# Kernel tuning notes

Hardware: AMD Instinct MI355X
Metric: run time of the kernel (lower is better)

Reference implementation:

```python
import jax, jax.numpy as jnp
import numpy as np

N, K, D_IN, D_OUT = 50000, 32, 128, 128
TEMPERATURE = 1.0


def setup_inputs() -> dict:
    key = jax.random.key(0)
    k1, k2, k3 = jax.random.split(key, 3)
    feat = jax.random.normal(k1, (N, D_IN), dtype=jnp.float32)
    # Glorot-like scale so pairwise distances stay in a reasonable softmax range
    weight = jax.random.normal(k2, (D_IN, D_OUT), dtype=jnp.float32) / np.sqrt(D_IN)
    bias = jnp.zeros((D_OUT,), dtype=jnp.float32)
    # norm='none' -> unit edge weights; fixed-degree-k graph -> topk returns all k neighbors
    top_k_weights = jnp.ones((N, K), dtype=jnp.float32)
    top_k_idx = jax.random.randint(k3, (N, K), 0, N, dtype=jnp.int64)
    return {"feat": feat, "weight": weight, "bias": bias,
            "top_k_weights": top_k_weights, "top_k_idx": top_k_idx}


def reference(feat, weight, bias, top_k_weights, top_k_idx):
    # Linear projection (self.weight): [n, d_out]
    h = feat @ weight
    # Gather top-k neighbor embeddings: [n, k, d]
    fk = h[top_k_idx]
    mask = top_k_idx == -1                      # [n, k] missing-neighbor mask
    w = jnp.where(mask, 0.0, top_k_weights)     # zero out missing weights

    # Pairwise Euclidean distances among each node's k neighbors: [n, k, k]
    # ||a-b|| = sqrt(|a|^2 + |b|^2 - 2 a.b); avoids materializing [n,k,k,d]
    sq = jnp.sum(fk * fk, axis=-1)                          # [n, k]
    gram = jnp.einsum('nkd,nmd->nkm', fk, fk)               # [n, k, k]
    d2 = sq[:, :, None] + sq[:, None, :] - 2.0 * gram
    d2 = jnp.maximum(d2, 0.0)
    dist = jnp.sqrt(jnp.where(d2 > 0.0, d2, 1.0))
    dist = jnp.where(d2 > 0.0, dist, 0.0)                   # zero for identical pts / -1 idx
    # zero entries for missing pairs (matches partial_distance_matrix semantics)
    pair_mask = mask[:, :, None] | mask[:, None, :]
    dist = jnp.where(pair_mask, 0.0, dist)

    # Weighted sum of distances over neighbors (medoid cost): [n, k]
    dagg = jnp.einsum('nm,nkm->nk', w, dist)
    big = jnp.finfo(dist.dtype).max
    dagg = jnp.where(mask | ~jnp.isfinite(dagg), big, dagg)

    # Soft medoid weights
    r = jax.nn.softmax(-dagg / TEMPERATURE, axis=-1)
    # with_weight_correction=True
    r = r * w
    r = r / jnp.sum(r, axis=-1, keepdims=True)
    r = jnp.where(mask, 0.0, r)

    # spmm over the reliable adjacency: [n, d_out]
    out = jnp.einsum('nk,nkd->nd', r, fk)
    return out + bias
```

## Files before the change

kernel.cpp:

```cpp
#include <hip/hip_runtime.h>
#include <math.h>


typedef __attribute__((ext_vector_type(2)))  _Float16 half2v;
typedef __attribute__((ext_vector_type(4)))  _Float16 half4v;
typedef __attribute__((ext_vector_type(8)))  _Float16 half8;
typedef __attribute__((ext_vector_type(2)))  float    f32x2;
typedef __attribute__((ext_vector_type(16))) float    f32x16;

#define NK   32
#define DIM  128
#define ROWB 272
#define WPB  3
#define GEMM_BLOCKS 512

__global__ __launch_bounds__(256) void gemm128(
    const float* __restrict__ A, const float* __restrict__ W,
    _Float16* __restrict__ Hq, int n)
{
    __shared__ __align__(16) char smem[32 * 528];

    const int tid  = threadIdx.x;
    const int lane = tid & 63;
    const int l31  = lane & 31;
    const int hf   = lane >> 5;
    const int t    = tid >> 6;
    const int col  = l31 + 32 * t;

    const int sr = tid >> 3;
    const int sc = tid & 7;

    half8 af[8];
#pragma unroll
    for (int s = 0; s < 8; ++s) {
        const float* wp = W + (size_t)(16 * s + 8 * hf) * 128 + col;
#pragma unroll
        for (int e = 0; e < 8; ++e)
            af[s][e] = (_Float16)wp[(size_t)e * 128];
    }

    const int ntiles = (n + 31) >> 5;
    for (int tile = blockIdx.x; tile < ntiles; tile += GEMM_BLOCKS) {
        const int row0 = tile * 32;

        __syncthreads();

        {
            int rr = row0 + sr; if (rr >= n) rr = n - 1;
            const float* src = A + (size_t)rr * 128 + 4 * sc;
            char* dst = smem + sr * 528 + 16 * sc;
#pragma unroll
            for (int i = 0; i < 4; ++i) {
                float4 v = *reinterpret_cast<const float4*>(src + 32 * i);
                *reinterpret_cast<float4*>(dst + 128 * i) = v;
            }
        }

        __syncthreads();

        f32x16 acc;
#pragma unroll
        for (int i = 0; i < 16; ++i) acc[i] = 0.0f;

        const char* myrow = smem + l31 * 528 + 32 * hf;
#pragma unroll
        for (int s = 0; s < 8; ++s) {
            float4 b0 = *reinterpret_cast<const float4*>(myrow + 64 * s);
            float4 b1 = *reinterpret_cast<const float4*>(myrow + 64 * s + 16);
            half8 bf;
            bf[0] = (_Float16)b0.x; bf[1] = (_Float16)b0.y;
            bf[2] = (_Float16)b0.z; bf[3] = (_Float16)b0.w;
            bf[4] = (_Float16)b1.x; bf[5] = (_Float16)b1.y;
            bf[6] = (_Float16)b1.z; bf[7] = (_Float16)b1.w;
            acc = __builtin_amdgcn_mfma_f32_32x32x16_f16(af[s], bf, acc, 0, 0, 0);
        }

        __syncthreads();

        {
            char* orow = smem + l31 * 272 + 64 * t + 8 * hf;
#pragma unroll
            for (int g = 0; g < 4; ++g) {
                half4v hv;
#pragma unroll
                for (int q = 0; q < 4; ++q) hv[q] = (_Float16)acc[4 * g + q];
                *reinterpret_cast<half4v*>(orow + 16 * g) = hv;
            }
        }

        __syncthreads();

        {
            const int orow = row0 + sr;
            if (orow < n) {
                const char* srcl = smem + sr * 272 + 16 * sc;
                _Float16*   dst  = Hq + (size_t)orow * 128 + 8 * sc;
#pragma unroll
                for (int i = 0; i < 2; ++i) {
                    half8 v = *reinterpret_cast<const half8*>(srcl + 128 * i);
                    __builtin_nontemporal_store(
                        v, reinterpret_cast<half8*>(dst + 64 * i));
                }
            }
        }
    }
}

__global__ __launch_bounds__(192, 4) void softk(
    const _Float16* __restrict__ hq, const float* __restrict__ bias,
    const float* __restrict__ tkw, const int* __restrict__ idx,
    float* __restrict__ out, int n)
{
    __shared__ __align__(16) char  fkT[WPB][NK * ROWB];
    __shared__ __align__(16) float rbuf[WPB][NK];

    const int w    = threadIdx.x >> 6;
    const int lane = threadIdx.x & 63;
    const int l31  = lane & 31;
    const int hf   = lane >> 5;
    const int g    = lane >> 4;
    const int m    = lane & 15;
    const int pbase = (lane & 32) + ((lane & 32) >> 3);

    char* fkw = &fkT[w][0];

    const int d0 = 2 * lane;
    const float2 bv = *reinterpret_cast<const float2*>(bias + d0);
    const float4* rb = reinterpret_cast<const float4*>(&rbuf[w][0]);
    const int wbase = ROWB * g + 16 * ((m + 4 * g) & 15);
    const int fbase = ROWB * l31;
    const int uc0   = 4 * hf + 16 * (l31 & 3);
    int eaddr[4];
#pragma unroll
    for (int p = 0; p < 4; ++p) eaddr[p] = 4 * ((lane + 16 * p) & 63);

    const int stride = gridDim.x * WPB;
    int nd = blockIdx.x * WPB + w;
    if (nd >= n) return;

    int   vid = idx[(size_t)nd * NK + l31];
    float tw  = tkw[(size_t)nd * NK + l31];
    int   mkc = (vid < 0) ? 1 : 0;
    float wc  = mkc ? 0.0f : tw;
    half8 gb[8];
    {
        int idr = mkc ? 0 : vid;
#pragma unroll
        for (int i = 0; i < 8; ++i) {
            int idg = __shfl(idr, 4 * i + g, 64);
            gb[i] = *reinterpret_cast<const half8*>(
                hq + (size_t)idg * DIM + 8 * m);
        }
    }

    while (true) {
        const int  ndn = nd + stride;
        const bool hn  = ndn < n;

        int vid_n = 0; float tw_n = 0.0f;
        if (hn) {
            vid_n = idx[(size_t)ndn * NK + l31];
            tw_n  = tkw[(size_t)ndn * NK + l31];
        }

#pragma unroll
        for (int i = 0; i < 8; ++i)
            *reinterpret_cast<half8*>(&fkw[1088 * i + wbase]) = gb[i];

        f32x16 acc;
#pragma unroll
        for (int i = 0; i < 16; ++i) acc[i] = 0.0f;
        float sqp = 0.0f;
        int u = uc0;
#pragma unroll
        for (int s = 0; s < 8; ++s) {
            half8 fr = *reinterpret_cast<const half8*>(&fkw[fbase + 4 * (u & 63)]);
            u += 8;
            acc = __builtin_amdgcn_mfma_f32_32x32x16_f16(fr, fr, acc, 0, 0, 0);
            const half2v* p2 = reinterpret_cast<const half2v*>(&fr);
#pragma unroll
            for (int q = 0; q < 4; ++q)
                sqp = __builtin_amdgcn_fdot2(p2[q], p2[q], sqp, false);
        }
        float sq = sqp + __shfl_xor(sqp, 32, 64);

        const int mk_n = (vid_n < 0) ? 1 : 0;
        half8 gb_n[8];
        if (hn) {
            int idr_n = mk_n ? 0 : vid_n;
#pragma unroll
            for (int i = 0; i < 8; ++i) {
                int idg = __shfl(idr_n, 4 * i + g, 64);
                gb_n[i] = *reinterpret_cast<const half8*>(
                    hq + (size_t)idg * DIM + 8 * m);
            }
        }

        {
            _Float16 shi = (_Float16)sq;
            _Float16 slo = (_Float16)(sq - (float)shi);
            _Float16 nh  = (_Float16)(-0.5f * (float)shi);
            _Float16 nl  = (_Float16)(-0.5f * (float)slo);
            _Float16 z   = (_Float16)0.0f, one = (_Float16)1.0f;
            half8 aext = {z, z, z, z, z, z, z, z};
            half8 bext = {z, z, z, z, z, z, z, z};
            if (hf == 0) {
                aext[0] = nh;  aext[1] = nl;  aext[2] = one; aext[3] = one;
                bext[0] = one; bext[1] = one; bext[2] = nh;  bext[3] = nl;
            }
            acc = __builtin_amdgcn_mfma_f32_32x32x16_f16(aext, bext, acc, 0, 0, 0);
        }

        float pt[4] = {0.0f, 0.0f, 0.0f, 0.0f};
#pragma unroll
        for (int reg = 0; reg < 16; ++reg) {
            const int c = (reg & 3) + 8 * (reg >> 2);
            float wr = __shfl(wc, pbase + c, 64);
            float d2 = fmaxf(-(acc[reg] + acc[reg]), 0.0f);
            float ds = (d2 > 1e-4f) ? __builtin_amdgcn_sqrtf(d2) : 0.0f;
            pt[reg & 3] = fmaf(wr, ds, pt[reg & 3]);
        }
        float part = (pt[0] + pt[1]) + (pt[2] + pt[3]);
        float sA = part + __shfl_xor(part, 32, 64);
        if (mkc || !(sA < 3.4028235e38f)) sA = 3.4028235e38f;

        float x  = -sA;
        float mx = x;
#pragma unroll
        for (int o = 16; o > 0; o >>= 1) mx = fmaxf(mx, __shfl_xor(mx, o, 32));
        float t  = __expf(x - mx) * wc;
        float st = t;
#pragma unroll
        for (int o = 16; o > 0; o >>= 1) st += __shfl_xor(st, o, 32);
        float r = t * __builtin_amdgcn_rcpf(st);

        rbuf[w][l31] = r;

        float o0 = 0.0f, o1 = 0.0f;
#pragma unroll
        for (int q = 0; q < 8; ++q) {
            float4 rv = rb[q];
            half2v h0 = *reinterpret_cast<const half2v*>(&fkw[ROWB * (4 * q + 0) + eaddr[0]]);
            half2v h1 = *reinterpret_cast<const half2v*>(&fkw[ROWB * (4 * q + 1) + eaddr[1]]);
            half2v h2 = *reinterpret_cast<const half2v*>(&fkw[ROWB * (4 * q + 2) + eaddr[2]]);
            half2v h3 = *reinterpret_cast<const half2v*>(&fkw[ROWB * (4 * q + 3) + eaddr[3]]);
            o0 = fmaf(rv.x, (float)h0[0], o0); o1 = fmaf(rv.x, (float)h0[1], o1);
            o0 = fmaf(rv.y, (float)h1[0], o0); o1 = fmaf(rv.y, (float)h1[1], o1);
            o0 = fmaf(rv.z, (float)h2[0], o0); o1 = fmaf(rv.z, (float)h2[1], o1);
            o0 = fmaf(rv.w, (float)h3[0], o0); o1 = fmaf(rv.w, (float)h3[1], o1);
        }
        f32x2 ov; ov[0] = o0 + bv.x; ov[1] = o1 + bv.y;
        __builtin_nontemporal_store(
            ov, reinterpret_cast<f32x2*>(out + (size_t)nd * DIM + d0));

        if (!hn) break;
        nd  = ndn;
        mkc = mk_n;
        wc  = mk_n ? 0.0f : tw_n;
#pragma unroll
        for (int i = 0; i < 8; ++i) gb[i] = gb_n[i];
    }
}

extern "C" void kernel_launch(void* const* d_in, const int* in_sizes, int n_in,
                              void* d_out, int out_size, void* d_ws, size_t ws_size,
                              hipStream_t stream) {
    const float* feat = (const float*)d_in[0];
    const float* W    = (const float*)d_in[1];
    const float* bias = (const float*)d_in[2];
    const float* tkw  = (const float*)d_in[3];
    const int*   idx  = (const int*)d_in[4];
    float* out = (float*)d_out;

    const int n = in_sizes[0] / DIM;
    _Float16* hq = (_Float16*)d_ws;

    const int sblocks = (n + 4 * WPB - 1) / (4 * WPB);

    gemm128<<<GEMM_BLOCKS, 256, 0, stream>>>(feat, W, hq, n);
    softk<<<sblocks, 192, 0, stream>>>(hq, bias, tkw, idx, out, n);
}
```

Measured before the change: 144.8 us.

## Use single-wave blocks for softk and read neighbor weights from LDS padding

The softk kernel goes from three waves per block to one wave per block, so each workgroup holds one shared-memory tile and the grid grows so each block processes about four nodes. The per-register weight shuffles in the distance aggregation are replaced by a store of each neighbor weight into the unused padding bytes of its LDS row, then LDS reads. Smaller blocks may schedule more flexibly and avoid cross-wave LDS grouping, but they add per-block launch overhead, and the LDS reads exchange cross-lane shuffle traffic for LDS traffic.

```diff
diff --git a/kernel.cpp b/kernel.cpp
--- a/kernel.cpp
+++ b/kernel.cpp
@@ -11,7 +11,6 @@
 #define NK   32
 #define DIM  128
 #define ROWB 272
-#define WPB  3
 #define GEMM_BLOCKS 512
 
 __global__ __launch_bounds__(256) void gemm128(
@@ -106,36 +105,33 @@
     }
 }
 
-__global__ __launch_bounds__(192, 4) void softk(
+__global__ __launch_bounds__(64, 4) void softk(
     const _Float16* __restrict__ hq, const float* __restrict__ bias,
     const float* __restrict__ tkw, const int* __restrict__ idx,
     float* __restrict__ out, int n)
 {
-    __shared__ __align__(16) char  fkT[WPB][NK * ROWB];
-    __shared__ __align__(16) float rbuf[WPB][NK];
-
-    const int w    = threadIdx.x >> 6;
-    const int lane = threadIdx.x & 63;
+    __shared__ __align__(16) char  fkT[NK * ROWB];
+    __shared__ __align__(16) float rbuf[NK];
+
+    const int lane = threadIdx.x;
     const int l31  = lane & 31;
     const int hf   = lane >> 5;
     const int g    = lane >> 4;
     const int m    = lane & 15;
-    const int pbase = (lane & 32) + ((lane & 32) >> 3);
-
-    char* fkw = &fkT[w][0];
 
     const int d0 = 2 * lane;
     const float2 bv = *reinterpret_cast<const float2*>(bias + d0);
-    const float4* rb = reinterpret_cast<const float4*>(&rbuf[w][0]);
+    const float4* rb = reinterpret_cast<const float4*>(&rbuf[0]);
     const int wbase = ROWB * g + 16 * ((m + 4 * g) & 15);
     const int fbase = ROWB * l31;
     const int uc0   = 4 * hf + 16 * (l31 & 3);
+    const int wpadb = 1088 * hf + 256;
     int eaddr[4];
 #pragma unroll
     for (int p = 0; p < 4; ++p) eaddr[p] = 4 * ((lane + 16 * p) & 63);
 
-    const int stride = gridDim.x * WPB;
-    int nd = blockIdx.x * WPB + w;
+    const int stride = gridDim.x;
+    int nd = blockIdx.x;
     if (nd >= n) return;
 
     int   vid = idx[(size_t)nd * NK + l31];
@@ -165,7 +161,8 @@
 
 #pragma unroll
         for (int i = 0; i < 8; ++i)
-            *reinterpret_cast<half8*>(&fkw[1088 * i + wbase]) = gb[i];
+            *reinterpret_cast<half8*>(&fkT[1088 * i + wbase]) = gb[i];
+        *reinterpret_cast<float*>(&fkT[ROWB * l31 + 256]) = wc;
 
         f32x16 acc;
 #pragma unroll
@@ -174,7 +171,7 @@
         int u = uc0;
 #pragma unroll
         for (int s = 0; s < 8; ++s) {
-            half8 fr = *reinterpret_cast<const half8*>(&fkw[fbase + 4 * (u & 63)]);
+            half8 fr = *reinterpret_cast<const half8*>(&fkT[fbase + 4 * (u & 63)]);
             u += 8;
             acc = __builtin_amdgcn_mfma_f32_32x32x16_f16(fr, fr, acc, 0, 0, 0);
             const half2v* p2 = reinterpret_cast<const half2v*>(&fr);
@@ -215,7 +212,7 @@
 #pragma unroll
         for (int reg = 0; reg < 16; ++reg) {
             const int c = (reg & 3) + 8 * (reg >> 2);
-            float wr = __shfl(wc, pbase + c, 64);
+            float wr = *reinterpret_cast<const float*>(&fkT[wpadb + 272 * c]);
             float d2 = fmaxf(-(acc[reg] + acc[reg]), 0.0f);
             float ds = (d2 > 1e-4f) ? __builtin_amdgcn_sqrtf(d2) : 0.0f;
             pt[reg & 3] = fmaf(wr, ds, pt[reg & 3]);
@@ -234,16 +231,16 @@
         for (int o = 16; o > 0; o >>= 1) st += __shfl_xor(st, o, 32);
         float r = t * __builtin_amdgcn_rcpf(st);
 
-        rbuf[w][l31] = r;
+        rbuf[l31] = r;
 
         float o0 = 0.0f, o1 = 0.0f;
 #pragma unroll
         for (int q = 0; q < 8; ++q) {
             float4 rv = rb[q];
-            half2v h0 = *reinterpret_cast<const half2v*>(&fkw[ROWB * (4 * q + 0) + eaddr[0]]);
-            half2v h1 = *reinterpret_cast<const half2v*>(&fkw[ROWB * (4 * q + 1) + eaddr[1]]);
-            half2v h2 = *reinterpret_cast<const half2v*>(&fkw[ROWB * (4 * q + 2) + eaddr[2]]);
-            half2v h3 = *reinterpret_cast<const half2v*>(&fkw[ROWB * (4 * q + 3) + eaddr[3]]);
+            half2v h0 = *reinterpret_cast<const half2v*>(&fkT[ROWB * (4 * q + 0) + eaddr[0]]);
+            half2v h1 = *reinterpret_cast<const half2v*>(&fkT[ROWB * (4 * q + 1) + eaddr[1]]);
+            half2v h2 = *reinterpret_cast<const half2v*>(&fkT[ROWB * (4 * q + 2) + eaddr[2]]);
+            half2v h3 = *reinterpret_cast<const half2v*>(&fkT[ROWB * (4 * q + 3) + eaddr[3]]);
             o0 = fmaf(rv.x, (float)h0[0], o0); o1 = fmaf(rv.x, (float)h0[1], o1);
             o0 = fmaf(rv.y, (float)h1[0], o0); o1 = fmaf(rv.y, (float)h1[1], o1);
             o0 = fmaf(rv.z, (float)h2[0], o0); o1 = fmaf(rv.z, (float)h2[1], o1);
@@ -275,8 +272,8 @@
     const int n = in_sizes[0] / DIM;
     _Float16* hq = (_Float16*)d_ws;
 
-    const int sblocks = (n + 4 * WPB - 1) / (4 * WPB);
+    const int sblocks = (n + 3) / 4;
 
     gemm128<<<GEMM_BLOCKS, 256, 0, stream>>>(feat, W, hq, n);
-    softk<<<sblocks, 192, 0, stream>>>(hq, bias, tkw, idx, out, n);
+    softk<<<sblocks, 64, 0, stream>>>(hq, bias, tkw, idx, out, n);
 }
```

After: 142.2 us. No clear change (-1.8%).
